# Optimization experiments

Hardware: AMD Instinct MI355X
Metric: run time of the kernel (lower is better)

The kernel has to match this reference:

```python
import jax, jax.numpy as jnp
import numpy as np

T = 2.0          # hardcoded in the original __init__ (ignores the arg)
EPSILON = 0.1
N_ITERS = 20     # sinkhorn_loss passes n_iters=20 to sinkhorn_normalized
SCALE = 0.001


def setup_inputs() -> dict:
    key = jax.random.key(0)
    k1, k2 = jax.random.split(key)
    B, N, C = 8, 1024, 64
    y_s = jax.random.normal(k1, (B, N, C), dtype=jnp.float32)
    y_t = jax.random.normal(k2, (B, N, C), dtype=jnp.float32)
    return {"y_s": y_s, "y_t": y_t}


def _sinkhorn_loss(x, y):
    # x, y: [N, C]. cdist p=1 -> [N, N]
    Wxy = jnp.sum(jnp.abs(x[:, None, :] - y[None, :, :]), axis=-1)  # [N, N]
    K = jnp.exp(-Wxy / EPSILON)

    def body(P, _):
        P = P / jnp.sum(P, axis=1, keepdims=True)  # row normalize
        P = P / jnp.sum(P, axis=0, keepdims=True)  # col normalize
        return P, None

    P, _ = jax.lax.scan(body, K, None, length=N_ITERS)
    return jnp.sum(P * Wxy)


def reference(y_s, y_t):
    # softmax over dim=1 (the N axis), exactly as nn.Softmax(dim=1) on [B,N,C]
    p_s = jax.nn.softmax(y_s / T, axis=1)
    p_t = jax.nn.softmax(y_t / T, axis=1)
    # original Python loop computes the loss per sample but OVERWRITES
    # emd_loss each iteration; lax.map mirrors the sequential per-sample
    # work, and we return only the last sample's loss (faithful to the bug).
    losses = jax.lax.map(lambda xy: _sinkhorn_loss(xy[0], xy[1]), (p_s, p_t))
    return SCALE * losses[-1]
```

## Files before the change

kernel.cpp:

```cpp
#include <hip/hip_runtime.h>


static constexpr int N = 1024;
static constexpr int C = 64;

static constexpr int WS_XS  = 0;
static constexpr int WS_YS  = 65536;
static constexpr int WS_K   = 131072;
static constexpr int WS_KT  = 1179648;
static constexpr int WS_U   = 2228224;
static constexpr int WS_V   = 2229248;
static constexpr int WS_P   = 2230272;
static constexpr int WS_BAR = 2230592;

typedef float f32x4 __attribute__((ext_vector_type(4)));

__device__ __forceinline__ float wsum(float v) {
    #pragma unroll
    for (int o = 32; o > 0; o >>= 1) v += __shfl_down(v, o, 64);
    return v;
}
__device__ __forceinline__ float wmax(float v) {
    #pragma unroll
    for (int o = 32; o > 0; o >>= 1) v = fmaxf(v, __shfl_down(v, o, 64));
    return v;
}

__device__ __forceinline__ float aload(float* p) {
    return __hip_atomic_load(p, __ATOMIC_RELAXED, __HIP_MEMORY_SCOPE_AGENT);
}
__device__ __forceinline__ void astore(float* p, float v) {
    __hip_atomic_store(p, v, __ATOMIC_RELAXED, __HIP_MEMORY_SCOPE_AGENT);
}

__device__ __forceinline__ void llc_load4(const float* p, f32x4& a0, f32x4& a1,
                                          f32x4& a2, f32x4& a3) {
    asm volatile(
        "global_load_dwordx4 %0, %4, off sc0 sc1\n\t"
        "global_load_dwordx4 %1, %4, off offset:1024 sc0 sc1\n\t"
        "global_load_dwordx4 %2, %4, off offset:2048 sc0 sc1\n\t"
        "global_load_dwordx4 %3, %4, off offset:3072 sc0 sc1\n\t"
        "s_waitcnt vmcnt(0)"
        : "=&v"(a0), "=&v"(a1), "=&v"(a2), "=&v"(a3)
        : "v"(p)
        : "memory");
}
__device__ __forceinline__ void llc_load1(const float* p, f32x4& a0) {
    asm volatile(
        "global_load_dwordx4 %0, %1, off sc0 sc1\n\t"
        "s_waitcnt vmcnt(0)"
        : "=&v"(a0) : "v"(p) : "memory");
}

__device__ __forceinline__ void gridbar64(unsigned* cnt, unsigned& bar) {
    __syncthreads();
    ++bar;
    if (threadIdx.x == 0) {
        __hip_atomic_fetch_add(cnt, 1u, __ATOMIC_RELAXED, __HIP_MEMORY_SCOPE_AGENT);
        while (__hip_atomic_load(cnt, __ATOMIC_RELAXED, __HIP_MEMORY_SCOPE_AGENT)
               < bar * 64u)
            __builtin_amdgcn_s_sleep(1);
    }
    asm volatile("" ::: "memory");
    __syncthreads();
}

__global__ void __launch_bounds__(256)
softmax_k(const float* __restrict__ ysrc, const float* __restrict__ ytrc,
          float* __restrict__ ws)
{
    __shared__ float sm[4];
    const int tid = threadIdx.x, bid = blockIdx.x;
    const int wid = tid >> 6, lane = tid & 63;
    const float* src = ((bid < C) ? ysrc : ytrc) + 7 * N * C;
    float* dst = ws + ((bid < C) ? WS_XS : WS_YS);
    const int c = bid & (C - 1);

    float vals[4];
    float m = -1e30f;
    #pragma unroll
    for (int q = 0; q < 4; ++q) {
        vals[q] = src[(q * 256 + tid) * C + c] * 0.5f;
        m = fmaxf(m, vals[q]);
    }
    m = wmax(m);
    if (lane == 0) sm[wid] = m;
    __syncthreads();
    m = fmaxf(fmaxf(sm[0], sm[1]), fmaxf(sm[2], sm[3]));
    float s = 0.f;
    #pragma unroll
    for (int q = 0; q < 4; ++q) { vals[q] = expf(vals[q] - m); s += vals[q]; }
    s = wsum(s);
    __syncthreads();
    if (lane == 0) sm[wid] = s;
    __syncthreads();
    s = sm[0] + sm[1] + sm[2] + sm[3];
    const float inv = 1.0f / s;
    #pragma unroll
    for (int q = 0; q < 4; ++q) dst[(q * 256 + tid) * C + c] = vals[q] * inv;
}

__global__ void __launch_bounds__(256)
buildK_k(float* __restrict__ ws)
{
    __shared__ float smem[5184];
    float* xs  = ws + WS_XS;
    float* ysm = ws + WS_YS;
    float* K   = ws + WS_K;
    float* KT  = ws + WS_KT;
    const int tid = threadIdx.x, bid = blockIdx.x;

    if (bid < 4) ws[WS_V + bid * 256 + tid] = 1.0f;
    if (bid == 0 && tid == 0) *(volatile unsigned*)(ws + WS_BAR) = 0u;

    float* sx = smem;
    float* sy = smem + 2048;
    float* kt = smem + 4128;
    #pragma unroll 1
    for (int t = 0; t < 4; ++t) {
        const int tt = bid * 4 + t;
        const int ti = tt >> 5, tj = tt & 31;
        __syncthreads();
        for (int k = tid; k < 2048; k += 256) sx[k] = xs[ti * 2048 + k];
        for (int k = tid; k < 2048; k += 256)
            sy[(k >> 6) * 65 + (k & 63)] = ysm[tj * 2048 + k];
        __syncthreads();
        float kv[4];
        #pragma unroll
        for (int q = 0; q < 4; ++q) {
            const int idx = q * 256 + tid;
            const int il = idx >> 5, jl = idx & 31;
            float a = 0.f;
            #pragma unroll
            for (int c2 = 0; c2 < 64; ++c2)
                a += fabsf(sx[il * 64 + c2] - sy[jl * 65 + c2]);
            kv[q] = expf(-10.0f * a);
            K[(ti * 32 + il) * N + tj * 32 + jl] = kv[q];
        }
        __syncthreads();
        #pragma unroll
        for (int q = 0; q < 4; ++q) {
            const int idx = q * 256 + tid;
            kt[(idx >> 5) * 33 + (idx & 31)] = kv[q];
        }
        __syncthreads();
        #pragma unroll
        for (int q = 0; q < 4; ++q) {
            const int idx = q * 256 + tid;
            const int jl = idx >> 5, il = idx & 31;
            KT[(tj * 32 + jl) * N + ti * 32 + il] = kt[il * 33 + jl];
        }
    }
}

__global__ void __launch_bounds__(256)
sinkhorn_loop_k(float* __restrict__ ws, float* __restrict__ out)
{
    __shared__ __align__(16) float rows[32 * 1024];
    __shared__ __align__(16) float sv[1024];
    __shared__ float fsm[4];
    const int tid = threadIdx.x, bid = blockIdx.x;
    const int wid = tid >> 6, lane = tid & 63;
    unsigned bar = 0;
    unsigned* cnt = (unsigned*)(ws + WS_BAR);

    {
        const f32x4* Ksrc  = (const f32x4*)(ws + WS_K  + bid * 16 * N);
        const f32x4* KTsrc = (const f32x4*)(ws + WS_KT + bid * 16 * N);
        f32x4* dK  = (f32x4*)rows;
        f32x4* dKT = (f32x4*)(rows + 16 * N);
        #pragma unroll 4
        for (int q = 0; q < 16; ++q) dK[tid + 256 * q]  = Ksrc[tid + 256 * q];
        #pragma unroll 4
        for (int q = 0; q < 16; ++q) dKT[tid + 256 * q] = KTsrc[tid + 256 * q];
    }
    __syncthreads();

    float* wsU = ws + WS_U;
    float* wsV = ws + WS_V;
    const float* myU = wsU + lane * 4;
    const float* myV = wsV + lane * 4;
    const int r0 = bid * 16 + wid * 4;
    const float* rK  = rows + (wid * 4) * N;
    const float* rKT = rows + 16 * N + (wid * 4) * N;
    float u_s[4];

    #pragma unroll 1
    for (int it = 0; it < 20; ++it) {
        f32x4 b0, b1, b2, b3;
        llc_load4(myV, b0, b1, b2, b3);
        #pragma unroll
        for (int s = 0; s < 4; ++s) {
            const f32x4* Kr = (const f32x4*)(rK + s * N);
            const f32x4 k0 = Kr[lane], k1 = Kr[lane + 64],
                        k2 = Kr[lane + 128], k3 = Kr[lane + 192];
            float acc = 0.f;
            acc += k0.x * b0.x + k0.y * b0.y + k0.z * b0.z + k0.w * b0.w;
            acc += k1.x * b1.x + k1.y * b1.y + k1.z * b1.z + k1.w * b1.w;
            acc += k2.x * b2.x + k2.y * b2.y + k2.z * b2.z + k2.w * b2.w;
            acc += k3.x * b3.x + k3.y * b3.y + k3.z * b3.z + k3.w * b3.w;
            acc = wsum(acc);
            if (lane == 0) { u_s[s] = 1.0f / acc; astore(wsU + r0 + s, u_s[s]); }
        }
        gridbar64(cnt, bar);

        llc_load4(myU, b0, b1, b2, b3);
        #pragma unroll
        for (int s = 0; s < 4; ++s) {
            const f32x4* Kr = (const f32x4*)(rKT + s * N);
            const f32x4 k0 = Kr[lane], k1 = Kr[lane + 64],
                        k2 = Kr[lane + 128], k3 = Kr[lane + 192];
            float acc = 0.f;
            acc += k0.x * b0.x + k0.y * b0.y + k0.z * b0.z + k0.w * b0.w;
            acc += k1.x * b1.x + k1.y * b1.y + k1.z * b1.z + k1.w * b1.w;
            acc += k2.x * b2.x + k2.y * b2.y + k2.z * b2.z + k2.w * b2.w;
            acc += k3.x * b3.x + k3.y * b3.y + k3.z * b3.z + k3.w * b3.w;
            acc = wsum(acc);
            if (lane == 0) astore(wsV + r0 + s, 1.0f / acc);
        }
        gridbar64(cnt, bar);
    }

    {
        f32x4 vv;
        llc_load1(wsV + tid * 4, vv);
        *(f32x4*)(sv + tid * 4) = vv;
    }
    __syncthreads();
    {
        float p = 0.f;
        #pragma unroll
        for (int s = 0; s < 4; ++s) {
            const float* Kr = rK + s * N;
            float acc = 0.f;
            for (int j = lane; j < N; j += 64) {
                const float kk = Kr[j];
                acc += kk * sv[j] * logf(kk);
            }
            acc = wsum(acc);
            if (lane == 0) p += u_s[s] * acc;
        }
        if (lane == 0) astore(ws + WS_P + bid * 4 + wid, p);
    }
    gridbar64(cnt, bar);

    if (bid == 0) {
        float acc = aload(ws + WS_P + tid);
        acc = wsum(acc);
        if (lane == 0) fsm[wid] = acc;
        __syncthreads();
        if (tid == 0)
            out[0] = -1e-4f * (fsm[0] + fsm[1] + fsm[2] + fsm[3]);
    }
}

extern "C" void kernel_launch(void* const* d_in, const int* in_sizes, int n_in,
                              void* d_out, int out_size, void* d_ws, size_t ws_size,
                              hipStream_t stream) {
    const float* y_s = (const float*)d_in[0];
    const float* y_t = (const float*)d_in[1];
    float* ws = (float*)d_ws;

    softmax_k<<<dim3(128), dim3(256), 0, stream>>>(y_s, y_t, ws);
    buildK_k<<<dim3(256), dim3(256), 0, stream>>>(ws);
    sinkhorn_loop_k<<<dim3(64), dim3(256), 0, stream>>>(ws, (float*)d_out);
}
```

Baseline: 206.9 us.

## Fuse softmax, K build and Sinkhorn loop into one persistent kernel with tree barrier

```diff
diff --git a/kernel.cpp b/kernel.cpp
--- a/kernel.cpp
+++ b/kernel.cpp
@@ -52,117 +52,120 @@
         : "=&v"(a0) : "v"(p) : "memory");
 }
 
-__device__ __forceinline__ void gridbar64(unsigned* cnt, unsigned& bar) {
-    __syncthreads();
-    ++bar;
+template <bool FENCE>
+__device__ __forceinline__ void treebar(unsigned* base, int grp,
+                                        unsigned gtarget, unsigned gtotal) {
+    __syncthreads();
     if (threadIdx.x == 0) {
-        __hip_atomic_fetch_add(cnt, 1u, __ATOMIC_RELAXED, __HIP_MEMORY_SCOPE_AGENT);
-        while (__hip_atomic_load(cnt, __ATOMIC_RELAXED, __HIP_MEMORY_SCOPE_AGENT)
-               < bar * 64u)
+        if (FENCE) __builtin_amdgcn_fence(__ATOMIC_RELEASE, "agent");
+        unsigned* gln = base + 32 + grp * 32;
+        unsigned my = __hip_atomic_fetch_add(gln, 1u, __ATOMIC_RELAXED,
+                                             __HIP_MEMORY_SCOPE_AGENT) + 1u;
+        if (my == gtarget)
+            __hip_atomic_fetch_add(base, 1u, __ATOMIC_RELAXED,
+                                   __HIP_MEMORY_SCOPE_AGENT);
+        while (__hip_atomic_load(base, __ATOMIC_RELAXED,
+                                 __HIP_MEMORY_SCOPE_AGENT) < gtotal)
             __builtin_amdgcn_s_sleep(1);
+        if (FENCE) __builtin_amdgcn_fence(__ATOMIC_ACQUIRE, "agent");
     }
     asm volatile("" ::: "memory");
     __syncthreads();
 }
 
 __global__ void __launch_bounds__(256)
-softmax_k(const float* __restrict__ ysrc, const float* __restrict__ ytrc,
-          float* __restrict__ ws)
-{
-    __shared__ float sm[4];
-    const int tid = threadIdx.x, bid = blockIdx.x;
-    const int wid = tid >> 6, lane = tid & 63;
-    const float* src = ((bid < C) ? ysrc : ytrc) + 7 * N * C;
-    float* dst = ws + ((bid < C) ? WS_XS : WS_YS);
-    const int c = bid & (C - 1);
-
-    float vals[4];
-    float m = -1e30f;
-    #pragma unroll
-    for (int q = 0; q < 4; ++q) {
-        vals[q] = src[(q * 256 + tid) * C + c] * 0.5f;
-        m = fmaxf(m, vals[q]);
-    }
-    m = wmax(m);
-    if (lane == 0) sm[wid] = m;
-    __syncthreads();
-    m = fmaxf(fmaxf(sm[0], sm[1]), fmaxf(sm[2], sm[3]));
-    float s = 0.f;
-    #pragma unroll
-    for (int q = 0; q < 4; ++q) { vals[q] = expf(vals[q] - m); s += vals[q]; }
-    s = wsum(s);
-    __syncthreads();
-    if (lane == 0) sm[wid] = s;
-    __syncthreads();
-    s = sm[0] + sm[1] + sm[2] + sm[3];
-    const float inv = 1.0f / s;
-    #pragma unroll
-    for (int q = 0; q < 4; ++q) dst[(q * 256 + tid) * C + c] = vals[q] * inv;
-}
-
-__global__ void __launch_bounds__(256)
-buildK_k(float* __restrict__ ws)
-{
-    __shared__ float smem[5184];
-    float* xs  = ws + WS_XS;
-    float* ysm = ws + WS_YS;
-    float* K   = ws + WS_K;
-    float* KT  = ws + WS_KT;
-    const int tid = threadIdx.x, bid = blockIdx.x;
-
-    if (bid < 4) ws[WS_V + bid * 256 + tid] = 1.0f;
-    if (bid == 0 && tid == 0) *(volatile unsigned*)(ws + WS_BAR) = 0u;
-
-    float* sx = smem;
-    float* sy = smem + 2048;
-    float* kt = smem + 4128;
-    #pragma unroll 1
-    for (int t = 0; t < 4; ++t) {
-        const int tt = bid * 4 + t;
-        const int ti = tt >> 5, tj = tt & 31;
-        __syncthreads();
-        for (int k = tid; k < 2048; k += 256) sx[k] = xs[ti * 2048 + k];
-        for (int k = tid; k < 2048; k += 256)
-            sy[(k >> 6) * 65 + (k & 63)] = ysm[tj * 2048 + k];
-        __syncthreads();
-        float kv[4];
-        #pragma unroll
-        for (int q = 0; q < 4; ++q) {
-            const int idx = q * 256 + tid;
-            const int il = idx >> 5, jl = idx & 31;
-            float a = 0.f;
-            #pragma unroll
-            for (int c2 = 0; c2 < 64; ++c2)
-                a += fabsf(sx[il * 64 + c2] - sy[jl * 65 + c2]);
-            kv[q] = expf(-10.0f * a);
-            K[(ti * 32 + il) * N + tj * 32 + jl] = kv[q];
-        }
-        __syncthreads();
-        #pragma unroll
-        for (int q = 0; q < 4; ++q) {
-            const int idx = q * 256 + tid;
-            kt[(idx >> 5) * 33 + (idx & 31)] = kv[q];
-        }
-        __syncthreads();
-        #pragma unroll
-        for (int q = 0; q < 4; ++q) {
-            const int idx = q * 256 + tid;
-            const int jl = idx >> 5, il = idx & 31;
-            KT[(tj * 32 + jl) * N + ti * 32 + il] = kt[il * 33 + jl];
-        }
-    }
-}
-
-__global__ void __launch_bounds__(256)
-sinkhorn_loop_k(float* __restrict__ ws, float* __restrict__ out)
+sinkhorn_fused(const float* __restrict__ ysrc, const float* __restrict__ ytrc,
+               float* __restrict__ ws, float* __restrict__ out)
 {
     __shared__ __align__(16) float rows[32 * 1024];
     __shared__ __align__(16) float sv[1024];
     __shared__ float fsm[4];
     const int tid = threadIdx.x, bid = blockIdx.x;
     const int wid = tid >> 6, lane = tid & 63;
-    unsigned bar = 0;
-    unsigned* cnt = (unsigned*)(ws + WS_BAR);
+    const int grp = bid >> 3;
+    unsigned* base = (unsigned*)(ws + WS_BAR);
+    unsigned gtarget = 0, gtotal = 0;
+
+    if (bid < 2 * C) {
+        const float* src = ((bid < C) ? ysrc : ytrc) + 7 * N * C;
+        float* dst = ws + ((bid < C) ? WS_XS : WS_YS);
+        const int c = bid & (C - 1);
+        float vals[4];
+        float m = -1e30f;
+        #pragma unroll
+        for (int q = 0; q < 4; ++q) {
+            vals[q] = src[(q * 256 + tid) * C + c] * 0.5f;
+            m = fmaxf(m, vals[q]);
+        }
+        m = wmax(m);
+        if (lane == 0) fsm[wid] = m;
+        __syncthreads();
+        m = fmaxf(fmaxf(fsm[0], fsm[1]), fmaxf(fsm[2], fsm[3]));
+        float s = 0.f;
+        #pragma unroll
+        for (int q = 0; q < 4; ++q) { vals[q] = expf(vals[q] - m); s += vals[q]; }
+        s = wsum(s);
+        __syncthreads();
+        if (lane == 0) fsm[wid] = s;
+        __syncthreads();
+        s = fsm[0] + fsm[1] + fsm[2] + fsm[3];
+        const float inv = 1.0f / s;
+        #pragma unroll
+        for (int q = 0; q < 4; ++q) dst[(q * 256 + tid) * C + c] = vals[q] * inv;
+    }
+    gtarget += 8; gtotal += 32;
+    treebar<true>(base, grp, gtarget, gtotal);
+
+    {
+        float* xs  = ws + WS_XS;
+        float* ysm = ws + WS_YS;
+        float* K   = ws + WS_K;
+        float* KT  = ws + WS_KT;
+        if (bid < 4) astore(ws + WS_V + bid * 256 + tid, 1.0f);
+
+        float* sx = rows;
+        float* sy = rows + 2048;
+        float* kt = rows + 4128;
+        #pragma unroll 1
+        for (int t = 0; t < 4; ++t) {
+            const int tt = bid * 4 + t;
+            const int ti = tt >> 5, tj = tt & 31;
+            __syncthreads();
+            for (int k = tid; k < 2048; k += 256) sx[k] = xs[ti * 2048 + k];
+            for (int k = tid; k < 2048; k += 256)
+                sy[(k >> 6) * 65 + (k & 63)] = ysm[tj * 2048 + k];
+            __syncthreads();
+            float kv[4];
+            #pragma unroll
+            for (int q = 0; q < 4; ++q) {
+                const int idx = q * 256 + tid;
+                const int il = idx >> 5, jl = idx & 31;
+                float a = 0.f;
+                #pragma unroll
+                for (int c2 = 0; c2 < 64; ++c2)
+                    a += fabsf(sx[il * 64 + c2] - sy[jl * 65 + c2]);
+                kv[q] = expf(-10.0f * a);
+                K[(ti * 32 + il) * N + tj * 32 + jl] = kv[q];
+            }
+            __syncthreads();
+            #pragma unroll
+            for (int q = 0; q < 4; ++q) {
+                const int idx = q * 256 + tid;
+                kt[(idx >> 5) * 33 + (idx & 31)] = kv[q];
+            }
+            __syncthreads();
+            #pragma unroll
+            for (int q = 0; q < 4; ++q) {
+                const int idx = q * 256 + tid;
+                const int jl = idx >> 5, il = idx & 31;
+                KT[(tj * 32 + jl) * N + ti * 32 + il] = kt[il * 33 + jl];
+            }
+        }
+    }
+    gtarget += 8; gtotal += 32;
+    treebar<true>(base, grp, gtarget, gtotal);
+
+    if (bid >= 64) return;
 
     {
         const f32x4* Ksrc  = (const f32x4*)(ws + WS_K  + bid * 16 * N);
@@ -202,7 +205,8 @@
             acc = wsum(acc);
             if (lane == 0) { u_s[s] = 1.0f / acc; astore(wsU + r0 + s, u_s[s]); }
         }
-        gridbar64(cnt, bar);
+        gtarget += 8; gtotal += 8;
+        treebar<false>(base, grp, gtarget, gtotal);
 
         llc_load4(myU, b0, b1, b2, b3);
         #pragma unroll
@@ -218,7 +222,8 @@
             acc = wsum(acc);
             if (lane == 0) astore(wsV + r0 + s, 1.0f / acc);
         }
-        gridbar64(cnt, bar);
+        gtarget += 8; gtotal += 8;
+        treebar<false>(base, grp, gtarget, gtotal);
     }
 
     {
@@ -242,7 +247,8 @@
         }
         if (lane == 0) astore(ws + WS_P + bid * 4 + wid, p);
     }
-    gridbar64(cnt, bar);
+    gtarget += 8; gtotal += 8;
+    treebar<false>(base, grp, gtarget, gtotal);
 
     if (bid == 0) {
         float acc = aload(ws + WS_P + tid);
@@ -261,7 +267,8 @@
     const float* y_t = (const float*)d_in[1];
     float* ws = (float*)d_ws;
 
-    softmax_k<<<dim3(128), dim3(256), 0, stream>>>(y_s, y_t, ws);
-    buildK_k<<<dim3(256), dim3(256), 0, stream>>>(ws);
-    sinkhorn_loop_k<<<dim3(64), dim3(256), 0, stream>>>(ws, (float*)d_out);
-}
+    hipMemsetAsync((char*)d_ws + (size_t)WS_BAR * sizeof(float), 0,
+                   33 * 128, stream);
+    sinkhorn_fused<<<dim3(256), dim3(256), 0, stream>>>(y_s, y_t, ws,
+                                                        (float*)d_out);
+}
```

Measured after the change: 245.2 us. +18.5%, slower.

## Replace grid barriers with flag-tagged LL value exchange between blocks

Applied to the files above, without the earlier changes.

```diff
diff --git a/kernel.cpp b/kernel.cpp
--- a/kernel.cpp
+++ b/kernel.cpp
@@ -8,12 +8,13 @@
 static constexpr int WS_YS  = 65536;
 static constexpr int WS_K   = 131072;
 static constexpr int WS_KT  = 1179648;
-static constexpr int WS_U   = 2228224;
-static constexpr int WS_V   = 2229248;
-static constexpr int WS_P   = 2230272;
-static constexpr int WS_BAR = 2230592;
-
-typedef float f32x4 __attribute__((ext_vector_type(4)));
+static constexpr int WS_ULL = 2228224;
+static constexpr int WS_VLL = 2230272;
+static constexpr int WS_PLL = 2232320;
+
+typedef float    f32x4 __attribute__((ext_vector_type(4)));
+typedef unsigned u32x4 __attribute__((ext_vector_type(4)));
+typedef unsigned u32x2 __attribute__((ext_vector_type(2)));
 
 __device__ __forceinline__ float wsum(float v) {
     #pragma unroll
@@ -26,43 +27,32 @@
     return v;
 }
 
-__device__ __forceinline__ float aload(float* p) {
-    return __hip_atomic_load(p, __ATOMIC_RELAXED, __HIP_MEMORY_SCOPE_AGENT);
-}
-__device__ __forceinline__ void astore(float* p, float v) {
-    __hip_atomic_store(p, v, __ATOMIC_RELAXED, __HIP_MEMORY_SCOPE_AGENT);
-}
-
-__device__ __forceinline__ void llc_load4(const float* p, f32x4& a0, f32x4& a1,
-                                          f32x4& a2, f32x4& a3) {
-    asm volatile(
-        "global_load_dwordx4 %0, %4, off sc0 sc1\n\t"
-        "global_load_dwordx4 %1, %4, off offset:1024 sc0 sc1\n\t"
-        "global_load_dwordx4 %2, %4, off offset:2048 sc0 sc1\n\t"
-        "global_load_dwordx4 %3, %4, off offset:3072 sc0 sc1\n\t"
-        "s_waitcnt vmcnt(0)"
-        : "=&v"(a0), "=&v"(a1), "=&v"(a2), "=&v"(a3)
-        : "v"(p)
-        : "memory");
-}
-__device__ __forceinline__ void llc_load1(const float* p, f32x4& a0) {
-    asm volatile(
-        "global_load_dwordx4 %0, %1, off sc0 sc1\n\t"
-        "s_waitcnt vmcnt(0)"
-        : "=&v"(a0) : "v"(p) : "memory");
-}
-
-__device__ __forceinline__ void gridbar64(unsigned* cnt, unsigned& bar) {
-    __syncthreads();
-    ++bar;
-    if (threadIdx.x == 0) {
-        __hip_atomic_fetch_add(cnt, 1u, __ATOMIC_RELAXED, __HIP_MEMORY_SCOPE_AGENT);
-        while (__hip_atomic_load(cnt, __ATOMIC_RELAXED, __HIP_MEMORY_SCOPE_AGENT)
-               < bar * 64u)
-            __builtin_amdgcn_s_sleep(1);
-    }
-    asm volatile("" ::: "memory");
-    __syncthreads();
+__device__ __forceinline__ void ll_write(float* unit, float val, unsigned g) {
+    u32x2 d;
+    d.x = __float_as_uint(val);
+    d.y = g;
+    asm volatile("global_store_dwordx2 %0, %1, off sc0 sc1"
+                 :: "v"(unit), "v"(d) : "memory");
+}
+
+__device__ __forceinline__ void ll_read4(const float* buf, unsigned g,
+                                         float* sv, int t) {
+    const float* p = buf + t * 8;
+    u32x4 a, b;
+    for (;;) {
+        asm volatile(
+            "global_load_dwordx4 %0, %2, off sc0 sc1\n\t"
+            "global_load_dwordx4 %1, %2, off offset:16 sc0 sc1\n\t"
+            "s_waitcnt vmcnt(0)"
+            : "=&v"(a), "=&v"(b) : "v"(p) : "memory");
+        if (a.y == g && a.w == g && b.y == g && b.w == g) break;
+        __builtin_amdgcn_s_sleep(1);
+    }
+    const int u0 = t * 4;
+    sv[u0 + 0] = __uint_as_float(a.x);
+    sv[u0 + 1] = __uint_as_float(a.z);
+    sv[u0 + 2] = __uint_as_float(b.x);
+    sv[u0 + 3] = __uint_as_float(b.z);
 }
 
 __global__ void __launch_bounds__(256)
@@ -110,8 +100,7 @@
     float* KT  = ws + WS_KT;
     const int tid = threadIdx.x, bid = blockIdx.x;
 
-    if (bid < 4) ws[WS_V + bid * 256 + tid] = 1.0f;
-    if (bid == 0 && tid == 0) *(volatile unsigned*)(ws + WS_BAR) = 0u;
+    if (bid < 4) ws[WS_VLL + (bid * 256 + tid) * 2] = 1.0f;
 
     float* sx = smem;
     float* sy = smem + 2048;
@@ -158,11 +147,10 @@
 {
     __shared__ __align__(16) float rows[32 * 1024];
     __shared__ __align__(16) float sv[1024];
+    __shared__ float stage[16];
     __shared__ float fsm[4];
     const int tid = threadIdx.x, bid = blockIdx.x;
     const int wid = tid >> 6, lane = tid & 63;
-    unsigned bar = 0;
-    unsigned* cnt = (unsigned*)(ws + WS_BAR);
 
     {
         const f32x4* Ksrc  = (const f32x4*)(ws + WS_K  + bid * 16 * N);
@@ -176,56 +164,64 @@
     }
     __syncthreads();
 
-    float* wsU = ws + WS_U;
-    float* wsV = ws + WS_V;
-    const float* myU = wsU + lane * 4;
-    const float* myV = wsV + lane * 4;
-    const int r0 = bid * 16 + wid * 4;
+    float* uLL = ws + WS_ULL;
+    float* vLL = ws + WS_VLL;
+    float* pLL = ws + WS_PLL;
     const float* rK  = rows + (wid * 4) * N;
     const float* rKT = rows + 16 * N + (wid * 4) * N;
     float u_s[4];
+    unsigned g = 0;
 
     #pragma unroll 1
     for (int it = 0; it < 20; ++it) {
-        f32x4 b0, b1, b2, b3;
-        llc_load4(myV, b0, b1, b2, b3);
+        ll_read4(vLL, g, sv, tid);
+        __syncthreads();
         #pragma unroll
         for (int s = 0; s < 4; ++s) {
             const f32x4* Kr = (const f32x4*)(rK + s * N);
             const f32x4 k0 = Kr[lane], k1 = Kr[lane + 64],
                         k2 = Kr[lane + 128], k3 = Kr[lane + 192];
+            const f32x4 b0 = *(const f32x4*)&sv[(lane) * 4];
+            const f32x4 b1 = *(const f32x4*)&sv[(lane + 64) * 4];
+            const f32x4 b2 = *(const f32x4*)&sv[(lane + 128) * 4];
+            const f32x4 b3 = *(const f32x4*)&sv[(lane + 192) * 4];
             float acc = 0.f;
             acc += k0.x * b0.x + k0.y * b0.y + k0.z * b0.z + k0.w * b0.w;
             acc += k1.x * b1.x + k1.y * b1.y + k1.z * b1.z + k1.w * b1.w;
             acc += k2.x * b2.x + k2.y * b2.y + k2.z * b2.z + k2.w * b2.w;
             acc += k3.x * b3.x + k3.y * b3.y + k3.z * b3.z + k3.w * b3.w;
             acc = wsum(acc);
-            if (lane == 0) { u_s[s] = 1.0f / acc; astore(wsU + r0 + s, u_s[s]); }
-        }
-        gridbar64(cnt, bar);
-
-        llc_load4(myU, b0, b1, b2, b3);
+            if (lane == 0) { u_s[s] = 1.0f / acc; stage[wid * 4 + s] = u_s[s]; }
+        }
+        __syncthreads();
+        ++g;
+        if (tid < 16) ll_write(uLL + (bid * 16 + tid) * 2, stage[tid], g);
+
+        ll_read4(uLL, g, sv, tid);
+        __syncthreads();
         #pragma unroll
         for (int s = 0; s < 4; ++s) {
             const f32x4* Kr = (const f32x4*)(rKT + s * N);
             const f32x4 k0 = Kr[lane], k1 = Kr[lane + 64],
                         k2 = Kr[lane + 128], k3 = Kr[lane + 192];
+            const f32x4 b0 = *(const f32x4*)&sv[(lane) * 4];
+            const f32x4 b1 = *(const f32x4*)&sv[(lane + 64) * 4];
+            const f32x4 b2 = *(const f32x4*)&sv[(lane + 128) * 4];
+            const f32x4 b3 = *(const f32x4*)&sv[(lane + 192) * 4];
             float acc = 0.f;
             acc += k0.x * b0.x + k0.y * b0.y + k0.z * b0.z + k0.w * b0.w;
             acc += k1.x * b1.x + k1.y * b1.y + k1.z * b1.z + k1.w * b1.w;
             acc += k2.x * b2.x + k2.y * b2.y + k2.z * b2.z + k2.w * b2.w;
             acc += k3.x * b3.x + k3.y * b3.y + k3.z * b3.z + k3.w * b3.w;
             acc = wsum(acc);
-            if (lane == 0) astore(wsV + r0 + s, 1.0f / acc);
-        }
-        gridbar64(cnt, bar);
-    }
-
-    {
-        f32x4 vv;
-        llc_load1(wsV + tid * 4, vv);
-        *(f32x4*)(sv + tid * 4) = vv;
-    }
+            if (lane == 0) stage[wid * 4 + s] = 1.0f / acc;
+        }
+        __syncthreads();
+        ++g;
+        if (tid < 16) ll_write(vLL + (bid * 16 + tid) * 2, stage[tid], g);
+    }
+
+    ll_read4(vLL, g, sv, tid);
     __syncthreads();
     {
         float p = 0.f;
@@ -240,12 +236,20 @@
             acc = wsum(acc);
             if (lane == 0) p += u_s[s] * acc;
         }
-        if (lane == 0) astore(ws + WS_P + bid * 4 + wid, p);
-    }
-    gridbar64(cnt, bar);
+        if (lane == 0) ll_write(pLL + (bid * 4 + wid) * 2, p, 41u);
+    }
 
     if (bid == 0) {
-        float acc = aload(ws + WS_P + tid);
+        const float* pp = pLL + tid * 2;
+        u32x2 c;
+        for (;;) {
+            asm volatile("global_load_dwordx2 %0, %1, off sc0 sc1\n\t"
+                         "s_waitcnt vmcnt(0)"
+                         : "=&v"(c) : "v"(pp) : "memory");
+            if (c.y == 41u) break;
+            __builtin_amdgcn_s_sleep(1);
+        }
+        float acc = __uint_as_float(c.x);
         acc = wsum(acc);
         if (lane == 0) fsm[wid] = acc;
         __syncthreads();
@@ -261,6 +265,8 @@
     const float* y_t = (const float*)d_in[1];
     float* ws = (float*)d_ws;
 
+    hipMemsetAsync((char*)d_ws + (size_t)WS_ULL * sizeof(float), 0,
+                   (size_t)(2048 + 2048 + 512) * sizeof(float), stream);
     softmax_k<<<dim3(128), dim3(256), 0, stream>>>(y_s, y_t, ws);
     buildK_k<<<dim3(256), dim3(256), 0, stream>>>(ws);
     sinkhorn_loop_k<<<dim3(64), dim3(256), 0, stream>>>(ws, (float*)d_out);
```

New measurement: 200.2 us. 1.03x faster.
